# Performance work log

Hardware: AMD Instinct MI355X
Metric: run time of the kernel (lower is better)

Reference implementation:

```python
import jax, jax.numpy as jnp
import numpy as np

N_HEADS = 8
D_MODEL = 128


def _mha(q, k, v, w_in, b_in, w_out, b_out):
    # torch nn.MultiheadAttention math. q: [..., Lq, D], k/v: [..., Lk, D]
    D = q.shape[-1]
    hd = D // N_HEADS
    wq, wk, wv = jnp.split(w_in, 3, axis=0)
    bq, bk, bv = jnp.split(b_in, 3)
    qh = (q @ wq.T + bq).reshape(*q.shape[:-1], N_HEADS, hd)
    kh = (k @ wk.T + bk).reshape(*k.shape[:-1], N_HEADS, hd)
    vh = (v @ wv.T + bv).reshape(*v.shape[:-1], N_HEADS, hd)
    scale = 1.0 / np.sqrt(hd).astype(np.float32)
    scores = jnp.einsum('...qhd,...khd->...hqk', qh, kh) * scale
    attn = jax.nn.softmax(scores, axis=-1)
    out = jnp.einsum('...hqk,...khd->...qhd', attn, vh)
    out = out.reshape(*out.shape[:-2], D)
    return out @ w_out.T + b_out


def setup_inputs() -> dict:
    key = jax.random.key(0)
    ks = jax.random.split(key, 10)
    B, T, M, D = 4, 64, 256, D_MODEL
    K = 4  # neighbors per route
    s = 0.02
    inp = {
        'x': jax.random.normal(ks[0], (B, T, M, D), dtype=jnp.float32),
        'route_neighbors': jax.random.randint(ks[1], (M, K), 0, M, dtype=jnp.int32),
        't_w_in': s * jax.random.normal(ks[2], (3 * D, D), dtype=jnp.float32),
        't_b_in': jnp.zeros((3 * D,), dtype=jnp.float32),
        't_w_out': s * jax.random.normal(ks[3], (D, D), dtype=jnp.float32),
        't_b_out': jnp.zeros((D,), dtype=jnp.float32),
        's_w_in': s * jax.random.normal(ks[4], (3 * D, D), dtype=jnp.float32),
        's_b_in': jnp.zeros((3 * D,), dtype=jnp.float32),
        's_w_out': s * jax.random.normal(ks[5], (D, D), dtype=jnp.float32),
        's_b_out': jnp.zeros((D,), dtype=jnp.float32),
    }
    return inp


def reference(x, route_neighbors, t_w_in, t_b_in, t_w_out, t_b_out,
              s_w_in, s_b_in, s_w_out, s_b_out):
    B, T, M, D = x.shape
    K = route_neighbors.shape[1]
    xm = jnp.swapaxes(x, 1, 2)  # [B, M, T, D]
    # Temporal self-attention: independent per (B, M) over time axis.
    t_out = _mha(xm, xm, xm, t_w_in, t_b_in, t_w_out, t_b_out)  # [B, M, T, D]
    # Spatial cross-route attention: each route's series attends over its
    # neighbors' full time series (keys stacked along sequence axis).
    kv = x[:, :, route_neighbors]                    # [B, T, M, K, D]
    kv = jnp.transpose(kv, (0, 2, 1, 3, 4)).reshape(B, M, T * K, D)
    s_out = _mha(xm, kv, kv, s_w_in, s_b_in, s_w_out, s_b_out)  # [B, M, T, D]
    return jnp.swapaxes(t_out + s_out, 1, 2)  # [B, T, M, D]
```

## Files before the change

kernel.cpp:

```cpp
#include <hip/hip_runtime.h>
#include <hip/hip_bf16.h>


typedef __attribute__((ext_vector_type(8))) short bf16x8;
typedef __attribute__((ext_vector_type(4))) short short4v;
typedef __attribute__((ext_vector_type(4))) float f32x4;

#define DEVI static __device__ __forceinline__
#define MFMA(a, b, c) __builtin_amdgcn_mfma_f32_16x16x32_bf16(a, b, c, 0, 0, 0)

static constexpr float QSCALE = 0.25f * 1.44269504088896340736f * 0.5f;

DEVI short f2bfs(float f) {
  __hip_bfloat16 h = __float2bfloat16(f);
  return __builtin_bit_cast(short, h);
}

DEVI int swzb(int row, int colh) {
  return (row * 256 + colh * 2) ^ ((row & 7) << 4);
}

__global__ void __launch_bounds__(256) k_prep(
    const float* __restrict__ twin, const float* __restrict__ tbin,
    const float* __restrict__ twout, const float* __restrict__ tbout,
    const float* __restrict__ swin, const float* __restrict__ sbin,
    const float* __restrict__ swout, const float* __restrict__ sbout,
    short* __restrict__ wcat, float* __restrict__ biasin,
    short* __restrict__ wto, short* __restrict__ wso, float* __restrict__ biasc) {
  const int stride = gridDim.x * 256;
  const int t0 = blockIdx.x * 256 + threadIdx.x;
  for (int i = t0; i < 768 * 128; i += stride) {
    float v = (i < 384 * 128) ? twin[i] : swin[i - 384 * 128];
    wcat[i] = f2bfs(v);
  }
  for (int i = t0; i < 128 * 128; i += stride) {
    wto[i] = f2bfs(twout[i]);
    wso[i] = f2bfs(swout[i]);
  }
  for (int i = t0; i < 768; i += stride)
    biasin[i] = (i < 384) ? tbin[i] : sbin[i - 384];
  for (int i = t0; i < 128; i += stride)
    biasc[i] = tbout[i] + sbout[i];
}

DEVI void attn_block(const char* qbuf, const char* kbuf, const char* vbuf,
                     int w, int lo, int hi, int colq,
                     f32x4 (*o)[4], float (*ls)[4]) {
  const f32x4 zf = {0.f, 0.f, 0.f, 0.f};
#pragma unroll
  for (int hh = 0; hh < 2; ++hh) {
    const int hc = (2 * w + hh) * 16;
    bf16x8 qf[4];
#pragma unroll
    for (int qt = 0; qt < 4; ++qt)
      qf[qt] = *(const bf16x8*)(qbuf + swzb(16 * qt + lo, hc + colq));
#pragma unroll
    for (int kc = 0; kc < 2; ++kc) {
      bf16x8 kf0 = *(const bf16x8*)(kbuf + swzb(16 * (2 * kc) + lo, hc + colq));
      bf16x8 kf1 = *(const bf16x8*)(kbuf + swzb(16 * (2 * kc + 1) + lo, hc + colq));
      f32x4 st0[4], st1[4];
#pragma unroll
      for (int qt = 0; qt < 4; ++qt) {
        st0[qt] = MFMA(kf0, qf[qt], zf);
        st1[qt] = MFMA(kf1, qf[qt], zf);
      }
#pragma unroll
      for (int qt = 0; qt < 4; ++qt)
#pragma unroll
        for (int r = 0; r < 4; ++r) {
          float p0 = exp2f(st0[qt][r]);
          float p1 = exp2f(st1[qt][r]);
          st0[qt][r] = p0; st1[qt][r] = p1;
          ls[hh][qt] += p0 + p1;
        }
      bf16x8 vf;
#pragma unroll
      for (int i = 0; i < 8; ++i) {
        int key = 32 * kc + 16 * (i >> 2) + 4 * hi + (i & 3);
        vf[i] = *(const short*)(vbuf + swzb(key, hc + lo));
      }
#pragma unroll
      for (int qt = 0; qt < 4; ++qt) {
        bf16x8 pa;
#pragma unroll
        for (int r = 0; r < 4; ++r) {
          pa[r] = f2bfs(st0[qt][r]);
          pa[4 + r] = f2bfs(st1[qt][r]);
        }
        o[hh][qt] = MFMA(pa, vf, o[hh][qt]);
      }
    }
  }
}

DEVI void outproj(const char* abuf, const short* __restrict__ wmat,
                  int w, int lo, int hi, f32x4* acc) {
#pragma unroll
  for (int kc = 0; kc < 4; ++kc) {
    bf16x8 a = *(const bf16x8*)(abuf + swzb(16 * w + lo, 32 * kc + 8 * hi));
#pragma unroll
    for (int ct = 0; ct < 8; ++ct) {
      bf16x8 bf = *(const bf16x8*)(wmat + (16 * ct + lo) * 128 + 32 * kc + 8 * hi);
      acc[ct] = MFMA(a, bf, acc[ct]);
    }
  }
}

__global__ void __launch_bounds__(256) k_fused_t(
    const float* __restrict__ x, const short* __restrict__ wcat,
    const float* __restrict__ biasin,
    short* __restrict__ sq, short* __restrict__ sk, short* __restrict__ sv,
    uint4* __restrict__ ot) {
  __shared__ uint4 smv[3072];
  char* bufX = (char*)smv;
  char* bufQ = bufX + 16384;
  char* bufK = bufX + 32768;
  const int bm = blockIdx.x, b = bm >> 8, m = bm & 255;
  const int tid = threadIdx.x;

#pragma unroll
  for (int it = 0; it < 8; ++it) {
    int li = it * 256 + tid;
    int row = li >> 5, c4 = li & 31;
    float4 v = reinterpret_cast<const float4*>(x)[(size_t)((b * 64 + row) * 256 + m) * 32 + c4];
    short4v s;
    s[0] = f2bfs(v.x); s[1] = f2bfs(v.y); s[2] = f2bfs(v.z); s[3] = f2bfs(v.w);
    *(short4v*)(bufX + swzb(row, c4 * 4)) = s;
  }
  __syncthreads();

  const int w = tid >> 6, lane = tid & 63, lo = lane & 15, hi = lane >> 4;
  const int colq = 8 * (hi & 1);
  const f32x4 zf = {0.f, 0.f, 0.f, 0.f};

  bf16x8 af[4][4];
#pragma unroll
  for (int kc = 0; kc < 4; ++kc)
#pragma unroll
    for (int rt = 0; rt < 4; ++rt)
      af[kc][rt] = *(const bf16x8*)(bufX + swzb(16 * rt + lo, 32 * kc + 8 * hi));
  __syncthreads();

#pragma unroll
  for (int p = 0; p < 6; ++p) {
#pragma unroll
    for (int j = 0; j < 2; ++j) {
      int ct = 2 * w + j;
      f32x4 a4[4] = {zf, zf, zf, zf};
#pragma unroll
      for (int kc = 0; kc < 4; ++kc) {
        bf16x8 bcol = *(const bf16x8*)(wcat + (p * 128 + 16 * ct + lo) * 128 + 32 * kc + 8 * hi);
#pragma unroll
        for (int rt = 0; rt < 4; ++rt) a4[rt] = MFMA(af[kc][rt], bcol, a4[rt]);
      }
      float bb = biasin[p * 128 + 16 * ct + lo];
      if (p < 3) {
        char* pb = (p == 0) ? bufQ : (p == 1) ? bufK : bufX;
        float sc = (p == 0) ? QSCALE : 1.0f;
#pragma unroll
        for (int rt = 0; rt < 4; ++rt)
#pragma unroll
          for (int r = 0; r < 4; ++r)
            *(short*)(pb + swzb(16 * rt + 4 * hi + r, 16 * ct + lo)) =
                f2bfs((a4[rt][r] + bb) * sc);
      } else {
        short* dst = (p == 3) ? sq : (p == 4) ? sk : sv;
        float sc = (p == 3) ? QSCALE : 1.0f;
#pragma unroll
        for (int rt = 0; rt < 4; ++rt)
#pragma unroll
          for (int r = 0; r < 4; ++r)
            dst[(size_t)(bm * 64 + 16 * rt + 4 * hi + r) * 128 + 16 * ct + lo] =
                f2bfs((a4[rt][r] + bb) * sc);
      }
    }
  }
  __syncthreads();

  f32x4 o_t[2][4];
  float ls_t[2][4];
#pragma unroll
  for (int hh = 0; hh < 2; ++hh)
#pragma unroll
    for (int qt = 0; qt < 4; ++qt) { o_t[hh][qt] = zf; ls_t[hh][qt] = 0.f; }
  attn_block(bufQ, bufK, bufX, w, lo, hi, colq, o_t, ls_t);
  __syncthreads();

#pragma unroll
  for (int hh = 0; hh < 2; ++hh) {
    const int hc = (2 * w + hh) * 16;
#pragma unroll
    for (int qt = 0; qt < 4; ++qt) {
      float l = ls_t[hh][qt];
      l += __shfl_xor(l, 16);
      l += __shfl_xor(l, 32);
      float linv = 1.0f / l;
#pragma unroll
      for (int r = 0; r < 4; ++r) {
        float lr = __shfl(linv, 4 * hi + r);
        *(short*)(bufQ + swzb(16 * qt + 4 * hi + r, hc + lo)) = f2bfs(o_t[hh][qt][r] * lr);
      }
    }
  }
  __syncthreads();
#pragma unroll
  for (int it = 0; it < 4; ++it) {
    int li = it * 256 + tid;
    ot[(size_t)bm * 1024 + li] = *(const uint4*)(bufQ + swzb(li >> 4, (li & 15) * 8));
  }
}

__global__ void __launch_bounds__(256, 3) k_attn_s(
    const short* __restrict__ sq, const short* __restrict__ skp,
    const short* __restrict__ svp, const int* __restrict__ route,
    short* __restrict__ os) {
  __shared__ char smem[32768];
  const int bm = blockIdx.x, b = bm >> 8, m = bm & 255;
  const int tid = threadIdx.x;
  const int w = tid >> 6;
  const int l = tid & 63;
  const int lo = l & 15, hi = l >> 4, hi1 = hi & 1;
  const int xr = (l & 3) ^ ((l >> 2) & 3);
  char* kbase = smem + w * 8192;
  char* vbase = kbase + 4096;
  const uint4* skp4 = (const uint4*)skp;
  const uint4* svp4 = (const uint4*)svp;
  const f32x4 zf = {0.f, 0.f, 0.f, 0.f};

  bf16x8 qf[2][4];
#pragma unroll
  for (int hh = 0; hh < 2; ++hh)
#pragma unroll
    for (int qt = 0; qt < 4; ++qt)
      qf[hh][qt] = *(const bf16x8*)(sq + (size_t)(bm * 64 + 16 * qt + lo) * 128 +
                                    w * 32 + hh * 16 + 8 * hi1);

  uint4 pk[4], pv[4];
  int nb = route[m * 4 + 0];

#define ISSUE()                                                            \
  do {                                                                     \
    size_t rb = ((size_t)((b * 256 + nb) * 64 + l)) * 16 + w * 4;          \
    _Pragma("unroll") for (int s = 0; s < 4; ++s) {                        \
      pk[s] = skp4[rb + s];                                                \
      pv[s] = svp4[rb + s];                                                \
    }                                                                      \
  } while (0)

#define WRITEKV()                                                          \
  do {                                                                     \
    _Pragma("unroll") for (int s = 0; s < 4; ++s) {                        \
      *(uint4*)(kbase + l * 64 + ((s ^ xr) * 16)) = pk[s];                 \
      *(uint4*)(vbase + l * 64 + s * 16) = pv[s];                          \
    }                                                                      \
  } while (0)

  ISSUE();
  WRITEKV();

  f32x4 o[2][4];
  float ls[2][4];
#pragma unroll
  for (int hh = 0; hh < 2; ++hh)
#pragma unroll
    for (int qt = 0; qt < 4; ++qt) { o[hh][qt] = zf; ls[hh][qt] = 0.f; }

  for (int c = 0; c < 4; ++c) {
    if (c < 3) { nb = route[m * 4 + c + 1]; ISSUE(); }
#pragma unroll
    for (int hh = 0; hh < 2; ++hh) {
      const int slotb = ((2 * hh + hi1) ^ xr) * 16;
      bf16x8 kf[4];
#pragma unroll
      for (int kt = 0; kt < 4; ++kt)
        kf[kt] = *(const bf16x8*)(kbase + (16 * kt + lo) * 64 + slotb);
#pragma unroll
      for (int kc = 0; kc < 2; ++kc) {
        f32x4 st0[4], st1[4];
#pragma unroll
        for (int qt = 0; qt < 4; ++qt) {
          st0[qt] = MFMA(kf[2 * kc], qf[hh][qt], zf);
          st1[qt] = MFMA(kf[2 * kc + 1], qf[hh][qt], zf);
        }
#pragma unroll
        for (int qt = 0; qt < 4; ++qt)
#pragma unroll
          for (int r = 0; r < 4; ++r) {
            float p0 = exp2f(st0[qt][r]);
            float p1 = exp2f(st1[qt][r]);
            st0[qt][r] = p0; st1[qt][r] = p1;
            ls[hh][qt] += p0 + p1;
          }
        bf16x8 vf;
#pragma unroll
        for (int i = 0; i < 8; ++i) {
          int key = 32 * kc + 16 * (i >> 2) + 4 * hi + (i & 3);
          vf[i] = *(const short*)(vbase + key * 64 + (hh * 16 + lo) * 2);
        }
#pragma unroll
        for (int qt = 0; qt < 4; ++qt) {
          bf16x8 pa;
#pragma unroll
          for (int r = 0; r < 4; ++r) {
            pa[r] = f2bfs(st0[qt][r]);
            pa[4 + r] = f2bfs(st1[qt][r]);
          }
          o[hh][qt] = MFMA(pa, vf, o[hh][qt]);
        }
      }
    }
    if (c < 3) WRITEKV();
  }

#pragma unroll
  for (int hh = 0; hh < 2; ++hh)
#pragma unroll
    for (int qt = 0; qt < 4; ++qt) {
      float lsum = ls[hh][qt];
      lsum += __shfl_xor(lsum, 16);
      lsum += __shfl_xor(lsum, 32);
      float linv = 1.0f / lsum;
#pragma unroll
      for (int r = 0; r < 4; ++r) {
        float lr = __shfl(linv, 4 * hi + r);
        *(short*)(kbase + (16 * qt + 4 * hi + r) * 64 + (hh * 16 + lo) * 2) =
            f2bfs(o[hh][qt][r] * lr);
      }
    }
#pragma unroll
  for (int s = 0; s < 4; ++s) {
    uint4 u = *(const uint4*)(kbase + l * 64 + s * 16);
    ((uint4*)os)[((size_t)(bm * 64 + l) * 128 + w * 32) / 8 + s] = u;
  }
#undef ISSUE
#undef WRITEKV
}

__global__ void __launch_bounds__(256) k_comb(
    const uint4* __restrict__ ot, const uint4* __restrict__ os,
    const short* __restrict__ wto, const short* __restrict__ wso,
    const float* __restrict__ biasc, float* __restrict__ out) {
  __shared__ uint4 smv[2048];
  char* bufT = (char*)smv;
  char* bufS = bufT + 16384;
  const int bm = blockIdx.x, b = bm >> 8, m = bm & 255;
  const int tid = threadIdx.x;
#pragma unroll
  for (int it = 0; it < 4; ++it) {
    int li = it * 256 + tid;
    int o_ = swzb(li >> 4, (li & 15) * 8);
    *(uint4*)(bufT + o_) = ot[(size_t)bm * 1024 + li];
    *(uint4*)(bufS + o_) = os[(size_t)bm * 1024 + li];
  }
  __syncthreads();
  const int w = tid >> 6, lane = tid & 63, lo = lane & 15, hi = lane >> 4;
  const f32x4 zf = {0.f, 0.f, 0.f, 0.f};
  f32x4 accT[8], accS[8];
#pragma unroll
  for (int ct = 0; ct < 8; ++ct) { accT[ct] = zf; accS[ct] = zf; }
  outproj(bufT, wto, w, lo, hi, accT);
  outproj(bufS, wso, w, lo, hi, accS);
#pragma unroll
  for (int ct = 0; ct < 8; ++ct) {
    float bb = biasc[16 * ct + lo];
#pragma unroll
    for (int r = 0; r < 4; ++r) {
      int t = 16 * w + 4 * hi + r;
      out[(size_t)((b * 64 + t) * 256 + m) * 128 + 16 * ct + lo] =
          accT[ct][r] + accS[ct][r] + bb;
    }
  }
}

extern "C" void kernel_launch(void* const* d_in, const int* in_sizes, int n_in,
                              void* d_out, int out_size, void* d_ws, size_t ws_size,
                              hipStream_t stream) {
  (void)in_sizes; (void)n_in; (void)out_size; (void)ws_size;
  const float* x = (const float*)d_in[0];
  const int* route = (const int*)d_in[1];
  const float* twin = (const float*)d_in[2];
  const float* tbin = (const float*)d_in[3];
  const float* twout = (const float*)d_in[4];
  const float* tbout = (const float*)d_in[5];
  const float* swin = (const float*)d_in[6];
  const float* sbin = (const float*)d_in[7];
  const float* swout = (const float*)d_in[8];
  const float* sbout = (const float*)d_in[9];

  char* ws = (char*)d_ws;
  size_t off = 0;
  auto alloc = [&](size_t bytes) {
    char* p = ws + off;
    off += (bytes + 255) & ~(size_t)255;
    return p;
  };
  short* wcat = (short*)alloc(768 * 128 * 2);
  float* biasin = (float*)alloc(768 * 4);
  short* wto = (short*)alloc(128 * 128 * 2);
  short* wso = (short*)alloc(128 * 128 * 2);
  float* biasc = (float*)alloc(128 * 4);
  short* sq = (short*)alloc((size_t)65536 * 128 * 2);
  short* sk = (short*)alloc((size_t)65536 * 128 * 2);
  short* sv = (short*)alloc((size_t)65536 * 128 * 2);
  uint4* ot = (uint4*)alloc((size_t)65536 * 128 * 2);
  short* os = (short*)alloc((size_t)65536 * 128 * 2);
  float* out = (float*)d_out;

  k_prep<<<dim3(64), dim3(256), 0, stream>>>(twin, tbin, twout, tbout, swin, sbin,
                                             swout, sbout, wcat, biasin, wto, wso, biasc);
  k_fused_t<<<dim3(1024), dim3(256), 0, stream>>>(x, wcat, biasin, sq, sk, sv, ot);
  k_attn_s<<<dim3(1024), dim3(256), 0, stream>>>(sq, sk, sv, route, os);
  k_comb<<<dim3(1024), dim3(256), 0, stream>>>(ot, (const uint4*)os, wto, wso, biasc, out);
}
```

Baseline: 155.2 us.

## Stream spatial-attention K tiles straight into LDS with double buffering

In the spatial attention kernel, K tiles for each neighbor are now loaded with global_load_lds directly into a double-buffered per-wave LDS region, so they no longer pass through registers. V still goes through registers but is written with a padded row stride of 72 bytes to reduce bank conflicts, and the chunk loop is fully unrolled. The output tile is now staged across waves and written to global memory in coalesced full rows after a block barrier. LDS use grows from 32KB to 50KB per block, which may cut occupancy below the requested 3 blocks per CU. Explicit vmcnt waits also serialise the V loads.

```diff
diff --git a/kernel.cpp b/kernel.cpp
--- a/kernel.cpp
+++ b/kernel.cpp
@@ -18,6 +18,16 @@
 
 DEVI int swzb(int row, int colh) {
   return (row * 256 + colh * 2) ^ ((row & 7) << 4);
+}
+
+DEVI unsigned ldsoff(const void* p) {
+  return (unsigned)(unsigned long long)(__attribute__((address_space(3))) const void*)p;
+}
+
+DEVI void gload16(const void* g, unsigned ldsByte) {
+  __builtin_amdgcn_global_load_lds(
+      (const __attribute__((address_space(1))) unsigned int*)g,
+      (__attribute__((address_space(3))) unsigned int*)ldsByte, 16, 0, 0);
 }
 
 __global__ void __launch_bounds__(256) k_prep(
@@ -213,17 +223,14 @@
 __global__ void __launch_bounds__(256, 3) k_attn_s(
     const short* __restrict__ sq, const short* __restrict__ skp,
     const short* __restrict__ svp, const int* __restrict__ route,
-    short* __restrict__ os) {
-  __shared__ char smem[32768];
+    uint4* __restrict__ os) {
+  __shared__ char smem[51200];
   const int bm = blockIdx.x, b = bm >> 8, m = bm & 255;
   const int tid = threadIdx.x;
-  const int w = tid >> 6;
-  const int l = tid & 63;
+  const int w = tid >> 6, l = tid & 63;
   const int lo = l & 15, hi = l >> 4, hi1 = hi & 1;
-  const int xr = (l & 3) ^ ((l >> 2) & 3);
-  char* kbase = smem + w * 8192;
-  char* vbase = kbase + 4096;
-  const uint4* skp4 = (const uint4*)skp;
+  char* wbase = smem + w * 12800;
+  const unsigned wb = ldsoff(wbase);
   const uint4* svp4 = (const uint4*)svp;
   const f32x4 zf = {0.f, 0.f, 0.f, 0.f};
 
@@ -235,28 +242,39 @@
       qf[hh][qt] = *(const bf16x8*)(sq + (size_t)(bm * 64 + 16 * qt + lo) * 128 +
                                     w * 32 + hh * 16 + 8 * hi1);
 
-  uint4 pk[4], pv[4];
+  uint4 pv[4];
+
+#define ISSUEK(BUF, NB)                                                       \
+  do {                                                                        \
+    const char* kb = (const char*)skp +                                       \
+                     ((size_t)((b * 256 + (NB)) * 64 + l)) * 256 + w * 64;    \
+    _Pragma("unroll") for (int s = 0; s < 4; ++s)                             \
+        gload16(kb + s * 16, wb + (BUF)*4096 + s * 1024);                     \
+  } while (0)
+
+#define ISSUEV(NB)                                                            \
+  do {                                                                        \
+    size_t rb = ((size_t)((b * 256 + (NB)) * 64 + l)) * 16 + w * 4;           \
+    _Pragma("unroll") for (int s = 0; s < 4; ++s) pv[s] = svp4[rb + s];       \
+  } while (0)
+
+#define WRITEV()                                                              \
+  do {                                                                        \
+    _Pragma("unroll") for (int s = 0; s < 4; ++s) {                           \
+      char* p = wbase + 8192 + l * 72 + s * 16;                               \
+      *(unsigned long long*)p =                                               \
+          ((unsigned long long)pv[s].y << 32) | pv[s].x;                      \
+      *(unsigned long long*)(p + 8) =                                         \
+          ((unsigned long long)pv[s].w << 32) | pv[s].z;                      \
+    }                                                                         \
+  } while (0)
+
   int nb = route[m * 4 + 0];
-
-#define ISSUE()                                                            \
-  do {                                                                     \
-    size_t rb = ((size_t)((b * 256 + nb) * 64 + l)) * 16 + w * 4;          \
-    _Pragma("unroll") for (int s = 0; s < 4; ++s) {                        \
-      pk[s] = skp4[rb + s];                                                \
-      pv[s] = svp4[rb + s];                                                \
-    }                                                                      \
-  } while (0)
-
-#define WRITEKV()                                                          \
-  do {                                                                     \
-    _Pragma("unroll") for (int s = 0; s < 4; ++s) {                        \
-      *(uint4*)(kbase + l * 64 + ((s ^ xr) * 16)) = pk[s];                 \
-      *(uint4*)(vbase + l * 64 + s * 16) = pv[s];                          \
-    }                                                                      \
-  } while (0)
-
-  ISSUE();
-  WRITEKV();
+  ISSUEK(0, nb);
+  ISSUEV(nb);
+  __builtin_amdgcn_sched_barrier(0);
+  asm volatile("s_waitcnt vmcnt(0)" ::: "memory");
+  WRITEV();
 
   f32x4 o[2][4];
   float ls[2][4];
@@ -265,15 +283,22 @@
 #pragma unroll
     for (int qt = 0; qt < 4; ++qt) { o[hh][qt] = zf; ls[hh][qt] = 0.f; }
 
+#pragma unroll
   for (int c = 0; c < 4; ++c) {
-    if (c < 3) { nb = route[m * 4 + c + 1]; ISSUE(); }
+    if (c < 3) {
+      nb = route[m * 4 + c + 1];
+      ISSUEK((c + 1) & 1, nb);
+      ISSUEV(nb);
+      __builtin_amdgcn_sched_barrier(0);
+    }
+    const char* kbuf = wbase + (c & 1) * 4096;
+    const char* vbuf = wbase + 8192;
 #pragma unroll
     for (int hh = 0; hh < 2; ++hh) {
-      const int slotb = ((2 * hh + hi1) ^ xr) * 16;
       bf16x8 kf[4];
 #pragma unroll
       for (int kt = 0; kt < 4; ++kt)
-        kf[kt] = *(const bf16x8*)(kbase + (16 * kt + lo) * 64 + slotb);
+        kf[kt] = *(const bf16x8*)(kbuf + (2 * hh + hi1) * 1024 + (16 * kt + lo) * 16);
 #pragma unroll
       for (int kc = 0; kc < 2; ++kc) {
         f32x4 st0[4], st1[4];
@@ -295,7 +320,7 @@
 #pragma unroll
         for (int i = 0; i < 8; ++i) {
           int key = 32 * kc + 16 * (i >> 2) + 4 * hi + (i & 3);
-          vf[i] = *(const short*)(vbase + key * 64 + (hh * 16 + lo) * 2);
+          vf[i] = *(const short*)(vbuf + key * 72 + (hh * 16 + lo) * 2);
         }
 #pragma unroll
         for (int qt = 0; qt < 4; ++qt) {
@@ -309,7 +334,10 @@
         }
       }
     }
-    if (c < 3) WRITEKV();
+    if (c < 3) {
+      asm volatile("s_waitcnt vmcnt(0)" ::: "memory");
+      WRITEV();
+    }
   }
 
 #pragma unroll
@@ -323,17 +351,21 @@
 #pragma unroll
       for (int r = 0; r < 4; ++r) {
         float lr = __shfl(linv, 4 * hi + r);
-        *(short*)(kbase + (16 * qt + 4 * hi + r) * 64 + (hh * 16 + lo) * 2) =
+        *(short*)(wbase + 8192 + (16 * qt + 4 * hi + r) * 64 + (hh * 16 + lo) * 2) =
             f2bfs(o[hh][qt][r] * lr);
       }
     }
-#pragma unroll
-  for (int s = 0; s < 4; ++s) {
-    uint4 u = *(const uint4*)(kbase + l * 64 + s * 16);
-    ((uint4*)os)[((size_t)(bm * 64 + l) * 128 + w * 32) / 8 + s] = u;
-  }
-#undef ISSUE
-#undef WRITEKV
+  __syncthreads();
+#pragma unroll
+  for (int it = 0; it < 4; ++it) {
+    int li = it * 256 + tid;
+    int row = li >> 4, q16 = li & 15;
+    const char* src = smem + (q16 >> 2) * 12800 + 8192 + row * 64 + (q16 & 3) * 16;
+    os[(size_t)bm * 1024 + li] = *(const uint4*)src;
+  }
+#undef ISSUEK
+#undef ISSUEV
+#undef WRITEV
 }
 
 __global__ void __launch_bounds__(256) k_comb(
@@ -403,12 +435,12 @@
   short* sk = (short*)alloc((size_t)65536 * 128 * 2);
   short* sv = (short*)alloc((size_t)65536 * 128 * 2);
   uint4* ot = (uint4*)alloc((size_t)65536 * 128 * 2);
-  short* os = (short*)alloc((size_t)65536 * 128 * 2);
+  uint4* os = (uint4*)alloc((size_t)65536 * 128 * 2);
   float* out = (float*)d_out;
 
   k_prep<<<dim3(64), dim3(256), 0, stream>>>(twin, tbin, twout, tbout, swin, sbin,
                                              swout, sbout, wcat, biasin, wto, wso, biasc);
   k_fused_t<<<dim3(1024), dim3(256), 0, stream>>>(x, wcat, biasin, sq, sk, sv, ot);
   k_attn_s<<<dim3(1024), dim3(256), 0, stream>>>(sq, sk, sv, route, os);
-  k_comb<<<dim3(1024), dim3(256), 0, stream>>>(ot, (const uint4*)os, wto, wso, biasc, out);
-}
+  k_comb<<<dim3(1024), dim3(256), 0, stream>>>(ot, os, wto, wso, biasc, out);
+}
```

Result: slower. 386.5 us (+149.1%).

## Store spatial K/V in per-warp blocked layout for coalesced neighbor loads

Applied to the files above, without the earlier changes.

The prep kernel now writes spatial K and V projections in a blocked layout grouped by 32-column slice (warp) and route, so each warp's neighbor tile is one contiguous 4KB chunk. The attention kernel's global loads become fully coalesced (lane-contiguous uint4 per step) instead of each lane reading a 64-byte strided piece. The LDS writes are remapped with a new swizzle to keep the same shared-memory layout for the MFMA reads. The neighbor loop is also fully unrolled, which may increase register pressure.

```diff
diff --git a/kernel.cpp b/kernel.cpp
--- a/kernel.cpp
+++ b/kernel.cpp
@@ -163,15 +163,22 @@
           for (int r = 0; r < 4; ++r)
             *(short*)(pb + swzb(16 * rt + 4 * hi + r, 16 * ct + lo)) =
                 f2bfs((a4[rt][r] + bb) * sc);
+      } else if (p == 3) {
+#pragma unroll
+        for (int rt = 0; rt < 4; ++rt)
+#pragma unroll
+          for (int r = 0; r < 4; ++r)
+            sq[(size_t)(bm * 64 + 16 * rt + 4 * hi + r) * 128 + 16 * ct + lo] =
+                f2bfs((a4[rt][r] + bb) * QSCALE);
       } else {
-        short* dst = (p == 3) ? sq : (p == 4) ? sk : sv;
-        float sc = (p == 3) ? QSCALE : 1.0f;
+        short* dst = (p == 4) ? sk : sv;
+        size_t blk = ((size_t)((ct >> 1) * 1024 + bm)) * 2048;
+        int qe = ((ct & 1) * 2 + (lo >> 3)) * 8 + (lo & 7);
 #pragma unroll
         for (int rt = 0; rt < 4; ++rt)
 #pragma unroll
           for (int r = 0; r < 4; ++r)
-            dst[(size_t)(bm * 64 + 16 * rt + 4 * hi + r) * 128 + 16 * ct + lo] =
-                f2bfs((a4[rt][r] + bb) * sc);
+            dst[blk + (16 * rt + 4 * hi + r) * 32 + qe] = f2bfs(a4[rt][r] + bb);
       }
     }
   }
@@ -217,10 +224,10 @@
   __shared__ char smem[32768];
   const int bm = blockIdx.x, b = bm >> 8, m = bm & 255;
   const int tid = threadIdx.x;
-  const int w = tid >> 6;
-  const int l = tid & 63;
+  const int w = tid >> 6, l = tid & 63;
   const int lo = l & 15, hi = l >> 4, hi1 = hi & 1;
   const int xr = (l & 3) ^ ((l >> 2) & 3);
+  const int sw = (l & 3) ^ ((l >> 2) & 3) ^ (l >> 4);
   char* kbase = smem + w * 8192;
   char* vbase = kbase + 4096;
   const uint4* skp4 = (const uint4*)skp;
@@ -240,18 +247,19 @@
 
 #define ISSUE()                                                            \
   do {                                                                     \
-    size_t rb = ((size_t)((b * 256 + nb) * 64 + l)) * 16 + w * 4;          \
+    size_t base = ((size_t)(w * 1024 + b * 256 + nb)) * 256;               \
     _Pragma("unroll") for (int s = 0; s < 4; ++s) {                        \
-      pk[s] = skp4[rb + s];                                                \
-      pv[s] = svp4[rb + s];                                                \
+      pk[s] = skp4[base + s * 64 + l];                                     \
+      pv[s] = svp4[base + s * 64 + l];                                     \
     }                                                                      \
   } while (0)
 
 #define WRITEKV()                                                          \
   do {                                                                     \
     _Pragma("unroll") for (int s = 0; s < 4; ++s) {                        \
-      *(uint4*)(kbase + l * 64 + ((s ^ xr) * 16)) = pk[s];                 \
-      *(uint4*)(vbase + l * 64 + s * 16) = pv[s];                          \
+      int kk = s * 16 + (l >> 2);                                          \
+      *(uint4*)(kbase + kk * 64 + sw * 16) = pk[s];                        \
+      *(uint4*)(vbase + kk * 64 + (l & 3) * 16) = pv[s];                   \
     }                                                                      \
   } while (0)
 
@@ -265,6 +273,7 @@
 #pragma unroll
     for (int qt = 0; qt < 4; ++qt) { o[hh][qt] = zf; ls[hh][qt] = 0.f; }
 
+#pragma unroll
   for (int c = 0; c < 4; ++c) {
     if (c < 3) { nb = route[m * 4 + c + 1]; ISSUE(); }
 #pragma unroll
```

Measured after the change: 396.6 us. 156% more time.
